# Performance work log

Measured on AMD Instinct MI355X. Metric: run time of the kernel, lower is better.

The kernel has to match this reference:

```python
import jax, jax.numpy as jnp
import numpy as np

N_NODES = 100000
N_EDGES = 1600000
IN_DIM = 256
HID = 64
OUT_DIM = 1
N_GRAPHS = 100


def setup_inputs() -> dict:
    key = jax.random.key(0)
    ks = jax.random.split(key, 12)
    x = jax.random.normal(ks[0], (N_NODES, IN_DIM), dtype=jnp.float32)
    edge_index = jax.random.randint(ks[1], (2, N_EDGES), 0, N_NODES, dtype=jnp.int64 if jax.config.read('jax_enable_x64') else jnp.int32)
    batch = jnp.sort(jax.random.randint(ks[2], (N_NODES,), 0, N_GRAPHS, dtype=jnp.int32))
    def lin(k, fan_in, fan_out):
        bound = 1.0 / np.sqrt(fan_in)
        kw, kb = jax.random.split(k)
        W = jax.random.uniform(kw, (fan_in, fan_out), minval=-bound, maxval=bound, dtype=jnp.float32)
        b = jax.random.uniform(kb, (fan_out,), minval=-bound, maxval=bound, dtype=jnp.float32)
        return W, b
    W1, b1 = lin(ks[3], IN_DIM, HID)
    W2, b2 = lin(ks[4], HID, HID)
    W3, b3 = lin(ks[5], HID, HID)
    Wl, bl = lin(ks[6], HID, OUT_DIM)
    return {"x": x, "edge_index": edge_index, "batch": batch,
            "W1": W1, "b1": b1, "W2": W2, "b2": b2, "W3": W3, "b3": b3,
            "Wl": Wl, "bl": bl}


def _gcn_layer(h, src, dst, norm, W, b):
    # PyG GCNConv: h' = scatter_add(norm * (h @ W)[src] -> dst) + b
    h = h @ W                                   # [N, F_out]
    msg = h[src] * norm[:, None]                # [E+N, F_out] irregular gather
    agg = jax.ops.segment_sum(msg, dst, num_segments=N_NODES)
    return agg + b


def reference(x, edge_index, batch, W1, b1, W2, b2, W3, b3, Wl, bl):
    # add self loops (static shape) as GCNConv does by default
    loops = jnp.arange(N_NODES, dtype=edge_index.dtype)
    src = jnp.concatenate([edge_index[0], loops])  # [E+N]
    dst = jnp.concatenate([edge_index[1], loops])  # [E+N]
    # symmetric normalization: deg over targets incl. self loops
    deg = jax.ops.segment_sum(jnp.ones_like(dst, dtype=x.dtype), dst, num_segments=N_NODES)
    dinv = jnp.where(deg > 0, jax.lax.rsqrt(deg), 0.0)
    norm = dinv[src] * dinv[dst]                # [E+N]

    h = jax.nn.relu(_gcn_layer(x, src, dst, norm, W1, b1))
    h = jax.nn.relu(_gcn_layer(h, src, dst, norm, W2, b2))
    h = _gcn_layer(h, src, dst, norm, W3, b3)   # last conv: no relu

    # global_add_pool over graphs; dropout is identity at inference
    pooled = jax.ops.segment_sum(h, batch, num_segments=N_GRAPHS)  # [G, HID]
    return pooled @ Wl + bl                     # [G, 1]
```

## Files before the change

kernel.cpp:

```cpp
#include <hip/hip_runtime.h>

#define N_NODES 100000
#define N_EDGES 1600000
#define IN_DIM 256
#define HID 64
#define N_GRAPHS 100
#define BSHIFT 8
#define NBUCK 391
#define CHUNK 4096
#define BCAP 5120

typedef __attribute__((ext_vector_type(8))) short short8;
typedef __attribute__((ext_vector_type(8))) unsigned short us8;
typedef __attribute__((ext_vector_type(4))) float floatx4;

__device__ __forceinline__ unsigned short f2b(float f) {
    unsigned int u = __float_as_uint(f);
    unsigned int r = (u + 0x7FFFu + ((u >> 16) & 1u)) >> 16;
    return (unsigned short)r;
}
__device__ __forceinline__ float b2f(unsigned short b) {
    return __uint_as_float(((unsigned int)b) << 16);
}


__global__ void k_prep(const float* __restrict__ W1, const float* __restrict__ W2,
                       const float* __restrict__ W3, const float* __restrict__ Wl,
                       const float* __restrict__ b3,
                       unsigned short* __restrict__ wt1, unsigned short* __restrict__ wt2,
                       float* __restrict__ w3l,
                       int* __restrict__ bcnt, float* __restrict__ partial) {
    int i = blockIdx.x * 256 + threadIdx.x;
    if (i < IN_DIM * HID) {
        int k = i >> 6, n = i & 63;
        wt1[n * IN_DIM + k] = f2b(W1[i]);
    }
    if (i < HID * HID) {
        int k = i >> 6, n = i & 63;
        wt2[n * HID + k] = f2b(W2[i]);
    }
    if (i < NBUCK) bcnt[i] = 0;
    if (i < N_GRAPHS * 256) partial[i] = 0.f;
    if (blockIdx.x == 0) {
        int t = threadIdx.x;
        if (t < HID) {
            float s = 0.f;
            for (int n = 0; n < HID; ++n) s += W3[t * HID + n] * Wl[n];
            w3l[t] = s;
        } else if (t == HID) {
            float s = 0.f;
            for (int n = 0; n < HID; ++n) s += b3[n] * Wl[n];
            w3l[HID] = s;
        }
    }
}


__global__ __launch_bounds__(256) void k_scatter(const int* __restrict__ src,
                                                 const int* __restrict__ dst,
                                                 int* __restrict__ bcnt,
                                                 int* __restrict__ ebuckF) {
    __shared__ int lc[NBUCK];
    const int b = blockIdx.x, t = threadIdx.x;
    for (int i = t; i < NBUCK; i += 256) lc[i] = 0;
    __syncthreads();
    const int base = b * CHUNK;
    int pk[16], bk[16], rk[16];
#pragma unroll
    for (int i = 0; i < 16; ++i) {
        int e = base + i * 256 + t;
        rk[i] = -1;
        if (e < N_EDGES) {
            int s = src[e], d = dst[e];
            bk[i] = d >> BSHIFT;
            pk[i] = (s << BSHIFT) | (d & 255);
            rk[i] = atomicAdd(&lc[bk[i]], 1);
        }
    }
    __syncthreads();
    for (int i = t; i < NBUCK; i += 256)
        lc[i] = lc[i] ? atomicAdd(&bcnt[i], lc[i]) : 0;
    __syncthreads();
#pragma unroll
    for (int i = 0; i < 16; ++i)
        if (rk[i] >= 0) {
            int p = lc[bk[i]] + rk[i];
            if (p < BCAP) ebuckF[bk[i] * BCAP + p] = pk[i];
        }
}


__global__ __launch_bounds__(256) void k_degfill(const int* __restrict__ bcnt,
                                                 const int* __restrict__ ebuckF,
                                                 int* __restrict__ deg,
                                                 float* __restrict__ dinv,
                                                 int* __restrict__ rowptr,
                                                 int* __restrict__ colF) {
    __shared__ int ld[256];
    __shared__ int sA[256];
    __shared__ int lf[256];
    const int b = blockIdx.x, t = threadIdx.x;
    const int cnt = min(bcnt[b], BCAP);
    const int ebase = b * BCAP;
    ld[t] = 1;
    __syncthreads();
    for (int j = t; j < cnt; j += 256) atomicAdd(&ld[ebuckF[ebase + j] & 255], 1);
    __syncthreads();
    const int node = (b << BSHIFT) + t;
    const int dg = ld[t];
    if (node < N_NODES) {
        deg[node] = dg;
        dinv[node] = rsqrtf((float)dg);
    }
    const int c = (node < N_NODES) ? dg - 1 : 0;
    sA[t] = c;
    __syncthreads();
    for (int off = 1; off < 256; off <<= 1) {
        int u = (t >= off) ? sA[t - off] : 0;
        __syncthreads();
        sA[t] += u;
        __syncthreads();
    }
    const int pos = ebase + sA[t] - c;
    if (node < N_NODES) rowptr[node] = pos;
    lf[t] = pos;
    __syncthreads();
    for (int j = t; j < cnt; j += 256) {
        int v = ebuckF[ebase + j];
        int p = atomicAdd(&lf[v & 255], 1);
        colF[p] = v >> BSHIFT;
    }
}


__global__ __launch_bounds__(256) void k_gemm1(const float* __restrict__ X,
                                               const unsigned short* __restrict__ Wt,
                                               const float* __restrict__ dinv,
                                               unsigned short* __restrict__ Tb) {
    __shared__ unsigned short Wb[64][264];
    const int t = threadIdx.x;
    const int lane = t & 63, wv = t >> 6;
    const int fl = lane & 15, quad = lane >> 4;
    const int r0 = blockIdx.x * 64;

    for (int g = t; g < 64 * 32; g += 256) {
        int n = g >> 5, kc8 = g & 31;
        *(us8*)&Wb[n][kc8 * 8] = *(const us8*)(Wt + n * IN_DIM + kc8 * 8);
    }

    const int arow = r0 + wv * 16 + fl;
    const bool valid = arow < N_NODES;
    const float* xp = X + (size_t)(valid ? arow : 0) * IN_DIM;

    floatx4 acc[4];
#pragma unroll
    for (int j = 0; j < 4; ++j) acc[j] = (floatx4){0.f, 0.f, 0.f, 0.f};

    __syncthreads();

#pragma unroll
    for (int kc = 0; kc < IN_DIM; kc += 32) {
        float4 x0 = make_float4(0.f, 0.f, 0.f, 0.f);
        float4 x1 = make_float4(0.f, 0.f, 0.f, 0.f);
        if (valid) {
            x0 = *(const float4*)(xp + kc + quad * 8);
            x1 = *(const float4*)(xp + kc + quad * 8 + 4);
        }
        short8 a;
        a[0] = (short)f2b(x0.x); a[1] = (short)f2b(x0.y);
        a[2] = (short)f2b(x0.z); a[3] = (short)f2b(x0.w);
        a[4] = (short)f2b(x1.x); a[5] = (short)f2b(x1.y);
        a[6] = (short)f2b(x1.z); a[7] = (short)f2b(x1.w);
#pragma unroll
        for (int ct = 0; ct < 4; ++ct) {
            short8 b = *(const short8*)&Wb[ct * 16 + fl][kc + quad * 8];
            acc[ct] = __builtin_amdgcn_mfma_f32_16x16x32_bf16(a, b, acc[ct], 0, 0, 0);
        }
    }

    int rbase = r0 + wv * 16 + quad * 4;
#pragma unroll
    for (int r = 0; r < 4; ++r) {
        int row = rbase + r;
        if (row < N_NODES) {
            float di = dinv[row];
#pragma unroll
            for (int ct = 0; ct < 4; ++ct)
                Tb[(size_t)row * HID + ct * 16 + fl] = f2b(di * acc[ct][r]);
        }
    }
}


__global__ __launch_bounds__(256) void k_gemm2(const unsigned short* __restrict__ Xin,
                                               const unsigned short* __restrict__ Wt,
                                               const float* __restrict__ dinv,
                                               unsigned short* __restrict__ Tb) {
    __shared__ unsigned short Wb[64][72];
    const int t = threadIdx.x;
    const int lane = t & 63, wv = t >> 6;
    const int fl = lane & 15, quad = lane >> 4;
    const int r0 = blockIdx.x * 64;

    for (int g = t; g < 64 * 8; g += 256) {
        int n = g >> 3, kc8 = g & 7;
        *(us8*)&Wb[n][kc8 * 8] = *(const us8*)(Wt + n * HID + kc8 * 8);
    }

    const int arow = r0 + wv * 16 + fl;
    const bool valid = arow < N_NODES;
    const unsigned short* xp = Xin + (size_t)(valid ? arow : 0) * HID;

    floatx4 acc[4];
#pragma unroll
    for (int j = 0; j < 4; ++j) acc[j] = (floatx4){0.f, 0.f, 0.f, 0.f};

    __syncthreads();

#pragma unroll
    for (int kc = 0; kc < HID; kc += 32) {
        short8 a = (short8){0, 0, 0, 0, 0, 0, 0, 0};
        if (valid) a = *(const short8*)(xp + kc + quad * 8);
#pragma unroll
        for (int ct = 0; ct < 4; ++ct) {
            short8 b = *(const short8*)&Wb[ct * 16 + fl][kc + quad * 8];
            acc[ct] = __builtin_amdgcn_mfma_f32_16x16x32_bf16(a, b, acc[ct], 0, 0, 0);
        }
    }

    int rbase = r0 + wv * 16 + quad * 4;
#pragma unroll
    for (int r = 0; r < 4; ++r) {
        int row = rbase + r;
        if (row < N_NODES) {
            float di = dinv[row];
#pragma unroll
            for (int ct = 0; ct < 4; ++ct)
                Tb[(size_t)row * HID + ct * 16 + fl] = f2b(di * acc[ct][r]);
        }
    }
}


__global__ __launch_bounds__(1024) void k_agg(const unsigned short* __restrict__ Tb,
                                              const int* __restrict__ rowptr,
                                              const int* __restrict__ deg,
                                              const float* __restrict__ dinv,
                                              const int* __restrict__ col,
                                              const float* __restrict__ bias,
                                              unsigned short* __restrict__ Hb) {
    int lane = threadIdx.x & 63;
    int node = blockIdx.x * 16 + (threadIdx.x >> 6);
    int grp = lane >> 3, fl = lane & 7;
    int e = __builtin_amdgcn_readfirstlane(rowptr[node]);
    int end = e + __builtin_amdgcn_readfirstlane(deg[node]) - 1;
    float a0 = 0.f, a1 = 0.f, a2 = 0.f, a3 = 0.f;
    float a4 = 0.f, a5 = 0.f, a6 = 0.f, a7 = 0.f;
    for (; e + 16 <= end; e += 16) {
        int s0 = col[e + grp];
        int s1 = col[e + 8 + grp];
        us8 t0 = *(const us8*)(Tb + (size_t)s0 * HID + fl * 8);
        us8 t1 = *(const us8*)(Tb + (size_t)s1 * HID + fl * 8);
        a0 += b2f(t0[0]) + b2f(t1[0]); a1 += b2f(t0[1]) + b2f(t1[1]);
        a2 += b2f(t0[2]) + b2f(t1[2]); a3 += b2f(t0[3]) + b2f(t1[3]);
        a4 += b2f(t0[4]) + b2f(t1[4]); a5 += b2f(t0[5]) + b2f(t1[5]);
        a6 += b2f(t0[6]) + b2f(t1[6]); a7 += b2f(t0[7]) + b2f(t1[7]);
    }
    for (; e + 8 <= end; e += 8) {
        int s = col[e + grp];
        us8 tv = *(const us8*)(Tb + (size_t)s * HID + fl * 8);
        a0 += b2f(tv[0]); a1 += b2f(tv[1]); a2 += b2f(tv[2]); a3 += b2f(tv[3]);
        a4 += b2f(tv[4]); a5 += b2f(tv[5]); a6 += b2f(tv[6]); a7 += b2f(tv[7]);
    }
    if (e + grp < end) {
        int s = col[e + grp];
        us8 tv = *(const us8*)(Tb + (size_t)s * HID + fl * 8);
        a0 += b2f(tv[0]); a1 += b2f(tv[1]); a2 += b2f(tv[2]); a3 += b2f(tv[3]);
        a4 += b2f(tv[4]); a5 += b2f(tv[5]); a6 += b2f(tv[6]); a7 += b2f(tv[7]);
    }
    a0 += __shfl_xor(a0, 8);  a1 += __shfl_xor(a1, 8);
    a2 += __shfl_xor(a2, 8);  a3 += __shfl_xor(a3, 8);
    a4 += __shfl_xor(a4, 8);  a5 += __shfl_xor(a5, 8);
    a6 += __shfl_xor(a6, 8);  a7 += __shfl_xor(a7, 8);
    a0 += __shfl_xor(a0, 16); a1 += __shfl_xor(a1, 16);
    a2 += __shfl_xor(a2, 16); a3 += __shfl_xor(a3, 16);
    a4 += __shfl_xor(a4, 16); a5 += __shfl_xor(a5, 16);
    a6 += __shfl_xor(a6, 16); a7 += __shfl_xor(a7, 16);
    a0 += __shfl_xor(a0, 32); a1 += __shfl_xor(a1, 32);
    a2 += __shfl_xor(a2, 32); a3 += __shfl_xor(a3, 32);
    a4 += __shfl_xor(a4, 32); a5 += __shfl_xor(a5, 32);
    a6 += __shfl_xor(a6, 32); a7 += __shfl_xor(a7, 32);
    us8 sv = *(const us8*)(Tb + (size_t)node * HID + fl * 8);
    a0 += b2f(sv[0]); a1 += b2f(sv[1]); a2 += b2f(sv[2]); a3 += b2f(sv[3]);
    a4 += b2f(sv[4]); a5 += b2f(sv[5]); a6 += b2f(sv[6]); a7 += b2f(sv[7]);
    float di = dinv[node];
    float4 b0 = *(const float4*)(bias + fl * 8);
    float4 b1v = *(const float4*)(bias + fl * 8 + 4);
    a0 = fmaxf(fmaf(di, a0, b0.x), 0.f);
    a1 = fmaxf(fmaf(di, a1, b0.y), 0.f);
    a2 = fmaxf(fmaf(di, a2, b0.z), 0.f);
    a3 = fmaxf(fmaf(di, a3, b0.w), 0.f);
    a4 = fmaxf(fmaf(di, a4, b1v.x), 0.f);
    a5 = fmaxf(fmaf(di, a5, b1v.y), 0.f);
    a6 = fmaxf(fmaf(di, a6, b1v.z), 0.f);
    a7 = fmaxf(fmaf(di, a7, b1v.w), 0.f);
    if (grp == 0) {
        us8 o;
        o[0] = f2b(a0); o[1] = f2b(a1); o[2] = f2b(a2); o[3] = f2b(a3);
        o[4] = f2b(a4); o[5] = f2b(a5); o[6] = f2b(a6); o[7] = f2b(a7);
        *(us8*)(Hb + (size_t)node * HID + fl * 8) = o;
    }
}


__global__ __launch_bounds__(1024) void k_agg_z(const unsigned short* __restrict__ Tb,
                                                const int* __restrict__ rowptr,
                                                const int* __restrict__ deg,
                                                const float* __restrict__ dinv,
                                                const int* __restrict__ col,
                                                const float* __restrict__ bias,
                                                const float* __restrict__ w3l,
                                                float* __restrict__ z) {
    int lane = threadIdx.x & 63;
    int node = blockIdx.x * 16 + (threadIdx.x >> 6);
    int grp = lane >> 3, fl = lane & 7;
    int e = __builtin_amdgcn_readfirstlane(rowptr[node]);
    int end = e + __builtin_amdgcn_readfirstlane(deg[node]) - 1;
    float a0 = 0.f, a1 = 0.f, a2 = 0.f, a3 = 0.f;
    float a4 = 0.f, a5 = 0.f, a6 = 0.f, a7 = 0.f;
    for (; e + 16 <= end; e += 16) {
        int s0 = col[e + grp];
        int s1 = col[e + 8 + grp];
        us8 t0 = *(const us8*)(Tb + (size_t)s0 * HID + fl * 8);
        us8 t1 = *(const us8*)(Tb + (size_t)s1 * HID + fl * 8);
        a0 += b2f(t0[0]) + b2f(t1[0]); a1 += b2f(t0[1]) + b2f(t1[1]);
        a2 += b2f(t0[2]) + b2f(t1[2]); a3 += b2f(t0[3]) + b2f(t1[3]);
        a4 += b2f(t0[4]) + b2f(t1[4]); a5 += b2f(t0[5]) + b2f(t1[5]);
        a6 += b2f(t0[6]) + b2f(t1[6]); a7 += b2f(t0[7]) + b2f(t1[7]);
    }
    for (; e + 8 <= end; e += 8) {
        int s = col[e + grp];
        us8 tv = *(const us8*)(Tb + (size_t)s * HID + fl * 8);
        a0 += b2f(tv[0]); a1 += b2f(tv[1]); a2 += b2f(tv[2]); a3 += b2f(tv[3]);
        a4 += b2f(tv[4]); a5 += b2f(tv[5]); a6 += b2f(tv[6]); a7 += b2f(tv[7]);
    }
    if (e + grp < end) {
        int s = col[e + grp];
        us8 tv = *(const us8*)(Tb + (size_t)s * HID + fl * 8);
        a0 += b2f(tv[0]); a1 += b2f(tv[1]); a2 += b2f(tv[2]); a3 += b2f(tv[3]);
        a4 += b2f(tv[4]); a5 += b2f(tv[5]); a6 += b2f(tv[6]); a7 += b2f(tv[7]);
    }
    a0 += __shfl_xor(a0, 8);  a1 += __shfl_xor(a1, 8);
    a2 += __shfl_xor(a2, 8);  a3 += __shfl_xor(a3, 8);
    a4 += __shfl_xor(a4, 8);  a5 += __shfl_xor(a5, 8);
    a6 += __shfl_xor(a6, 8);  a7 += __shfl_xor(a7, 8);
    a0 += __shfl_xor(a0, 16); a1 += __shfl_xor(a1, 16);
    a2 += __shfl_xor(a2, 16); a3 += __shfl_xor(a3, 16);
    a4 += __shfl_xor(a4, 16); a5 += __shfl_xor(a5, 16);
    a6 += __shfl_xor(a6, 16); a7 += __shfl_xor(a7, 16);
    a0 += __shfl_xor(a0, 32); a1 += __shfl_xor(a1, 32);
    a2 += __shfl_xor(a2, 32); a3 += __shfl_xor(a3, 32);
    a4 += __shfl_xor(a4, 32); a5 += __shfl_xor(a5, 32);
    a6 += __shfl_xor(a6, 32); a7 += __shfl_xor(a7, 32);
    us8 sv = *(const us8*)(Tb + (size_t)node * HID + fl * 8);
    a0 += b2f(sv[0]); a1 += b2f(sv[1]); a2 += b2f(sv[2]); a3 += b2f(sv[3]);
    a4 += b2f(sv[4]); a5 += b2f(sv[5]); a6 += b2f(sv[6]); a7 += b2f(sv[7]);
    float di = dinv[node];
    float4 b0 = *(const float4*)(bias + fl * 8);
    float4 b1v = *(const float4*)(bias + fl * 8 + 4);
    a0 = fmaxf(fmaf(di, a0, b0.x), 0.f);
    a1 = fmaxf(fmaf(di, a1, b0.y), 0.f);
    a2 = fmaxf(fmaf(di, a2, b0.z), 0.f);
    a3 = fmaxf(fmaf(di, a3, b0.w), 0.f);
    a4 = fmaxf(fmaf(di, a4, b1v.x), 0.f);
    a5 = fmaxf(fmaf(di, a5, b1v.y), 0.f);
    a6 = fmaxf(fmaf(di, a6, b1v.z), 0.f);
    a7 = fmaxf(fmaf(di, a7, b1v.w), 0.f);
    float4 w0 = *(const float4*)(w3l + fl * 8);
    float4 w1v = *(const float4*)(w3l + fl * 8 + 4);
    float s = a0 * w0.x + a1 * w0.y + a2 * w0.z + a3 * w0.w +
              a4 * w1v.x + a5 * w1v.y + a6 * w1v.z + a7 * w1v.w;
    s += __shfl_xor(s, 1);
    s += __shfl_xor(s, 2);
    s += __shfl_xor(s, 4);
    if (lane == 0) z[node] = di * s;
}

__global__ __launch_bounds__(256) void k_aggpool_s(const float* __restrict__ z,
                                                   const int* __restrict__ rowptr,
                                                   const int* __restrict__ deg,
                                                   const float* __restrict__ dinv,
                                                   const int* __restrict__ col,
                                                   const float* __restrict__ w3l,
                                                   const int* __restrict__ batch,
                                                   float* __restrict__ partial) {
    int i = blockIdx.x * 256 + threadIdx.x;
    if (i >= N_NODES) return;
    int e = rowptr[i];
    int end = e + deg[i] - 1;
    float s0 = z[i], s1 = 0.f, s2 = 0.f, s3 = 0.f;
    for (; e + 4 <= end; e += 4) {
        s0 += z[col[e]];
        s1 += z[col[e + 1]];
        s2 += z[col[e + 2]];
        s3 += z[col[e + 3]];
    }
    for (; e < end; ++e) s0 += z[col[e]];
    float s = w3l[HID] + dinv[i] * (s0 + s1 + s2 + s3);
    atomicAdd(&partial[batch[i] * 256 + (blockIdx.x & 255)], s);
}

__global__ void k_pool_reduce(const float* __restrict__ partial,
                              const float* __restrict__ bl,
                              float* __restrict__ out) {
    int g = blockIdx.x, t = threadIdx.x;
    float s = partial[g * 256 + t];
    s += __shfl_xor(s, 32);
    s += __shfl_xor(s, 16);
    s += __shfl_xor(s, 8);
    s += __shfl_xor(s, 4);
    s += __shfl_xor(s, 2);
    s += __shfl_xor(s, 1);
    __shared__ float ws[4];
    if ((t & 63) == 0) ws[t >> 6] = s;
    __syncthreads();
    if (t == 0) out[g] = bl[0] + ws[0] + ws[1] + ws[2] + ws[3];
}

extern "C" void kernel_launch(void* const* d_in, const int* in_sizes, int n_in,
                              void* d_out, int out_size, void* d_ws, size_t ws_size,
                              hipStream_t stream) {
    const float* x     = (const float*)d_in[0];
    const int*   ei    = (const int*)d_in[1];
    const int*   batch = (const int*)d_in[2];
    const float* W1    = (const float*)d_in[3];
    const float* b1    = (const float*)d_in[4];
    const float* W2    = (const float*)d_in[5];
    const float* b2    = (const float*)d_in[6];
    const float* W3    = (const float*)d_in[7];
    const float* b3    = (const float*)d_in[8];
    const float* Wl    = (const float*)d_in[9];
    const float* bl    = (const float*)d_in[10];
    float* out = (float*)d_out;

    char* p = (char*)d_ws;
    unsigned short* tb = (unsigned short*)p; p += (size_t)N_NODES * HID * 2;
    unsigned short* hB = (unsigned short*)p; p += (size_t)N_NODES * HID * 2;
    int*   colF    = (int*)p;   p += (size_t)NBUCK * BCAP * 4;
    int*   ebuckF  = (int*)p;   p += (size_t)NBUCK * BCAP * 4;
    int*   deg     = (int*)p;   p += (size_t)N_NODES * 4;
    float* dinv    = (float*)p; p += (size_t)N_NODES * 4;
    int*   rowptr  = (int*)p;   p += (size_t)N_NODES * 4;
    float* z       = (float*)p; p += (size_t)N_NODES * 4;
    int*   bcnt    = (int*)p;   p += (NBUCK + 1) * 4;
    float* partial = (float*)p; p += (size_t)N_GRAPHS * 256 * 4;
    unsigned short* wt1 = (unsigned short*)p; p += (size_t)IN_DIM * HID * 2;
    unsigned short* wt2 = (unsigned short*)p; p += (size_t)HID * HID * 2;
    float* w3l     = (float*)p; p += 128 * 4;

    const int* src  = ei;
    const int* dstp = ei + N_EDGES;

    const int nb = (N_NODES + 255) / 256;
    const int cb = (N_EDGES + CHUNK - 1) / CHUNK;
    const int gemm_blocks = (N_NODES + 63) / 64;
    const int agg_blocks = (N_NODES + 15) / 16;

    k_prep<<<128, 256, 0, stream>>>(W1, W2, W3, Wl, b3, wt1, wt2, w3l, bcnt, partial);
    k_scatter<<<cb, 256, 0, stream>>>(src, dstp, bcnt, ebuckF);
    k_degfill<<<NBUCK, 256, 0, stream>>>(bcnt, ebuckF, deg, dinv, rowptr, colF);

    k_gemm1<<<gemm_blocks, 256, 0, stream>>>(x, wt1, dinv, tb);
    k_agg<<<agg_blocks, 1024, 0, stream>>>(tb, rowptr, deg, dinv, colF, b1, hB);
    k_gemm2<<<gemm_blocks, 256, 0, stream>>>(hB, wt2, dinv, tb);
    k_agg_z<<<agg_blocks, 1024, 0, stream>>>(tb, rowptr, deg, dinv, colF, b2, w3l, z);

    k_aggpool_s<<<nb, 256, 0, stream>>>(z, rowptr, deg, dinv, colF, w3l, batch, partial);
    k_pool_reduce<<<N_GRAPHS, 256, 0, stream>>>(partial, bl, out);
}
```

Measured before the change: 365.6 us.

## Replace bucketed CSR build with fixed-capacity per-node adjacency and fuse agg with gemm2

Replaces the two-pass bucket scatter and degree/prefix-sum fill with a single atomic scatter into a fixed 64-slot adjacency list per destination node, computing the normalisation from the counts wherever it is needed. It also fuses the layer-1 aggregation with the layer-2 GEMM in one kernel that stages 16 aggregated rows in shared memory for a single wave's MFMA. This drops two graph-build kernels and the separate GEMM launch with its round trip of hidden features. In exchange it uses a global atomic per edge, edges beyond 64 per node are silently dropped, and the MFMA stage runs on only one wave per block.

```diff
diff --git a/kernel.cpp b/kernel.cpp
--- a/kernel.cpp
+++ b/kernel.cpp
@@ -5,10 +5,7 @@
 #define IN_DIM 256
 #define HID 64
 #define N_GRAPHS 100
-#define BSHIFT 8
-#define NBUCK 391
-#define CHUNK 4096
-#define BCAP 5120
+#define NCAP 64
 
 typedef __attribute__((ext_vector_type(8))) short short8;
 typedef __attribute__((ext_vector_type(8))) unsigned short us8;
@@ -24,12 +21,16 @@
 }
 
 
-__global__ void k_prep(const float* __restrict__ W1, const float* __restrict__ W2,
-                       const float* __restrict__ W3, const float* __restrict__ Wl,
-                       const float* __restrict__ b3,
-                       unsigned short* __restrict__ wt1, unsigned short* __restrict__ wt2,
-                       float* __restrict__ w3l,
-                       int* __restrict__ bcnt, float* __restrict__ partial) {
+__global__ __launch_bounds__(256) void k_prep(const float* __restrict__ W1,
+                                              const float* __restrict__ W2,
+                                              const float* __restrict__ W3,
+                                              const float* __restrict__ Wl,
+                                              const float* __restrict__ b3,
+                                              unsigned short* __restrict__ wt1,
+                                              unsigned short* __restrict__ wt2,
+                                              float* __restrict__ w3l,
+                                              int* __restrict__ ncnt,
+                                              float* __restrict__ partial) {
     int i = blockIdx.x * 256 + threadIdx.x;
     if (i < IN_DIM * HID) {
         int k = i >> 6, n = i & 63;
@@ -39,7 +40,7 @@
         int k = i >> 6, n = i & 63;
         wt2[n * HID + k] = f2b(W2[i]);
     }
-    if (i < NBUCK) bcnt[i] = 0;
+    if (i < N_NODES) ncnt[i] = 0;
     if (i < N_GRAPHS * 256) partial[i] = 0.f;
     if (blockIdx.x == 0) {
         int t = threadIdx.x;
@@ -56,86 +57,26 @@
 }
 
 
-__global__ __launch_bounds__(256) void k_scatter(const int* __restrict__ src,
-                                                 const int* __restrict__ dst,
-                                                 int* __restrict__ bcnt,
-                                                 int* __restrict__ ebuckF) {
-    __shared__ int lc[NBUCK];
-    const int b = blockIdx.x, t = threadIdx.x;
-    for (int i = t; i < NBUCK; i += 256) lc[i] = 0;
-    __syncthreads();
-    const int base = b * CHUNK;
-    int pk[16], bk[16], rk[16];
-#pragma unroll
-    for (int i = 0; i < 16; ++i) {
-        int e = base + i * 256 + t;
-        rk[i] = -1;
+__global__ __launch_bounds__(256) void k_dscatter(const int* __restrict__ src,
+                                                  const int* __restrict__ dst,
+                                                  int* __restrict__ ncnt,
+                                                  int* __restrict__ col) {
+    int base = blockIdx.x * 1024 + threadIdx.x;
+#pragma unroll
+    for (int i = 0; i < 4; ++i) {
+        int e = base + i * 256;
         if (e < N_EDGES) {
-            int s = src[e], d = dst[e];
-            bk[i] = d >> BSHIFT;
-            pk[i] = (s << BSHIFT) | (d & 255);
-            rk[i] = atomicAdd(&lc[bk[i]], 1);
-        }
-    }
-    __syncthreads();
-    for (int i = t; i < NBUCK; i += 256)
-        lc[i] = lc[i] ? atomicAdd(&bcnt[i], lc[i]) : 0;
-    __syncthreads();
-#pragma unroll
-    for (int i = 0; i < 16; ++i)
-        if (rk[i] >= 0) {
-            int p = lc[bk[i]] + rk[i];
-            if (p < BCAP) ebuckF[bk[i] * BCAP + p] = pk[i];
-        }
-}
-
-
-__global__ __launch_bounds__(256) void k_degfill(const int* __restrict__ bcnt,
-                                                 const int* __restrict__ ebuckF,
-                                                 int* __restrict__ deg,
-                                                 float* __restrict__ dinv,
-                                                 int* __restrict__ rowptr,
-                                                 int* __restrict__ colF) {
-    __shared__ int ld[256];
-    __shared__ int sA[256];
-    __shared__ int lf[256];
-    const int b = blockIdx.x, t = threadIdx.x;
-    const int cnt = min(bcnt[b], BCAP);
-    const int ebase = b * BCAP;
-    ld[t] = 1;
-    __syncthreads();
-    for (int j = t; j < cnt; j += 256) atomicAdd(&ld[ebuckF[ebase + j] & 255], 1);
-    __syncthreads();
-    const int node = (b << BSHIFT) + t;
-    const int dg = ld[t];
-    if (node < N_NODES) {
-        deg[node] = dg;
-        dinv[node] = rsqrtf((float)dg);
-    }
-    const int c = (node < N_NODES) ? dg - 1 : 0;
-    sA[t] = c;
-    __syncthreads();
-    for (int off = 1; off < 256; off <<= 1) {
-        int u = (t >= off) ? sA[t - off] : 0;
-        __syncthreads();
-        sA[t] += u;
-        __syncthreads();
-    }
-    const int pos = ebase + sA[t] - c;
-    if (node < N_NODES) rowptr[node] = pos;
-    lf[t] = pos;
-    __syncthreads();
-    for (int j = t; j < cnt; j += 256) {
-        int v = ebuckF[ebase + j];
-        int p = atomicAdd(&lf[v & 255], 1);
-        colF[p] = v >> BSHIFT;
+            int d = dst[e];
+            int slot = atomicAdd(&ncnt[d], 1);
+            if (slot < NCAP) col[(size_t)d * NCAP + slot] = src[e];
+        }
     }
 }
 
 
 __global__ __launch_bounds__(256) void k_gemm1(const float* __restrict__ X,
                                                const unsigned short* __restrict__ Wt,
-                                               const float* __restrict__ dinv,
+                                               const int* __restrict__ ncnt,
                                                unsigned short* __restrict__ Tb) {
     __shared__ unsigned short Wb[64][264];
     const int t = threadIdx.x;
@@ -183,7 +124,7 @@
     for (int r = 0; r < 4; ++r) {
         int row = rbase + r;
         if (row < N_NODES) {
-            float di = dinv[row];
+            float di = rsqrtf((float)(min(ncnt[row], NCAP) + 1));
 #pragma unroll
             for (int ct = 0; ct < 4; ++ct)
                 Tb[(size_t)row * HID + ct * 16 + fl] = f2b(di * acc[ct][r]);
@@ -192,68 +133,124 @@
 }
 
 
-__global__ __launch_bounds__(256) void k_gemm2(const unsigned short* __restrict__ Xin,
-                                               const unsigned short* __restrict__ Wt,
-                                               const float* __restrict__ dinv,
-                                               unsigned short* __restrict__ Tb) {
+__global__ __launch_bounds__(1024) void k_aggmm2(const unsigned short* __restrict__ Tb,
+                                                 const int* __restrict__ ncnt,
+                                                 const int* __restrict__ col,
+                                                 const float* __restrict__ bias,
+                                                 const unsigned short* __restrict__ Wt,
+                                                 unsigned short* __restrict__ Tb2) {
     __shared__ unsigned short Wb[64][72];
+    __shared__ unsigned short Hs[16][72];
     const int t = threadIdx.x;
     const int lane = t & 63, wv = t >> 6;
-    const int fl = lane & 15, quad = lane >> 4;
-    const int r0 = blockIdx.x * 64;
-
-    for (int g = t; g < 64 * 8; g += 256) {
+    const int grp = lane >> 3, fl8 = lane & 7;
+
+    for (int g = t; g < 64 * 8; g += 1024) {
         int n = g >> 3, kc8 = g & 7;
         *(us8*)&Wb[n][kc8 * 8] = *(const us8*)(Wt + n * HID + kc8 * 8);
     }
 
-    const int arow = r0 + wv * 16 + fl;
-    const bool valid = arow < N_NODES;
-    const unsigned short* xp = Xin + (size_t)(valid ? arow : 0) * HID;
-
-    floatx4 acc[4];
-#pragma unroll
-    for (int j = 0; j < 4; ++j) acc[j] = (floatx4){0.f, 0.f, 0.f, 0.f};
-
+    const int node = blockIdx.x * 16 + wv;
+    const int cnt = min(__builtin_amdgcn_readfirstlane(ncnt[node]), NCAP);
+    int e = node * NCAP;
+    const int end = e + cnt;
+    float a0 = 0.f, a1 = 0.f, a2 = 0.f, a3 = 0.f;
+    float a4 = 0.f, a5 = 0.f, a6 = 0.f, a7 = 0.f;
+    for (; e + 16 <= end; e += 16) {
+        int s0 = col[e + grp];
+        int s1 = col[e + 8 + grp];
+        us8 t0 = *(const us8*)(Tb + (size_t)s0 * HID + fl8 * 8);
+        us8 t1 = *(const us8*)(Tb + (size_t)s1 * HID + fl8 * 8);
+        a0 += b2f(t0[0]) + b2f(t1[0]); a1 += b2f(t0[1]) + b2f(t1[1]);
+        a2 += b2f(t0[2]) + b2f(t1[2]); a3 += b2f(t0[3]) + b2f(t1[3]);
+        a4 += b2f(t0[4]) + b2f(t1[4]); a5 += b2f(t0[5]) + b2f(t1[5]);
+        a6 += b2f(t0[6]) + b2f(t1[6]); a7 += b2f(t0[7]) + b2f(t1[7]);
+    }
+    for (; e + 8 <= end; e += 8) {
+        int s = col[e + grp];
+        us8 tv = *(const us8*)(Tb + (size_t)s * HID + fl8 * 8);
+        a0 += b2f(tv[0]); a1 += b2f(tv[1]); a2 += b2f(tv[2]); a3 += b2f(tv[3]);
+        a4 += b2f(tv[4]); a5 += b2f(tv[5]); a6 += b2f(tv[6]); a7 += b2f(tv[7]);
+    }
+    if (e + grp < end) {
+        int s = col[e + grp];
+        us8 tv = *(const us8*)(Tb + (size_t)s * HID + fl8 * 8);
+        a0 += b2f(tv[0]); a1 += b2f(tv[1]); a2 += b2f(tv[2]); a3 += b2f(tv[3]);
+        a4 += b2f(tv[4]); a5 += b2f(tv[5]); a6 += b2f(tv[6]); a7 += b2f(tv[7]);
+    }
+    a0 += __shfl_xor(a0, 8);  a1 += __shfl_xor(a1, 8);
+    a2 += __shfl_xor(a2, 8);  a3 += __shfl_xor(a3, 8);
+    a4 += __shfl_xor(a4, 8);  a5 += __shfl_xor(a5, 8);
+    a6 += __shfl_xor(a6, 8);  a7 += __shfl_xor(a7, 8);
+    a0 += __shfl_xor(a0, 16); a1 += __shfl_xor(a1, 16);
+    a2 += __shfl_xor(a2, 16); a3 += __shfl_xor(a3, 16);
+    a4 += __shfl_xor(a4, 16); a5 += __shfl_xor(a5, 16);
+    a6 += __shfl_xor(a6, 16); a7 += __shfl_xor(a7, 16);
+    a0 += __shfl_xor(a0, 32); a1 += __shfl_xor(a1, 32);
+    a2 += __shfl_xor(a2, 32); a3 += __shfl_xor(a3, 32);
+    a4 += __shfl_xor(a4, 32); a5 += __shfl_xor(a5, 32);
+    a6 += __shfl_xor(a6, 32); a7 += __shfl_xor(a7, 32);
+    us8 sv = *(const us8*)(Tb + (size_t)node * HID + fl8 * 8);
+    a0 += b2f(sv[0]); a1 += b2f(sv[1]); a2 += b2f(sv[2]); a3 += b2f(sv[3]);
+    a4 += b2f(sv[4]); a5 += b2f(sv[5]); a6 += b2f(sv[6]); a7 += b2f(sv[7]);
+    float di = rsqrtf((float)(cnt + 1));
+    float4 b0 = *(const float4*)(bias + fl8 * 8);
+    float4 b1v = *(const float4*)(bias + fl8 * 8 + 4);
+    a0 = fmaxf(fmaf(di, a0, b0.x), 0.f);
+    a1 = fmaxf(fmaf(di, a1, b0.y), 0.f);
+    a2 = fmaxf(fmaf(di, a2, b0.z), 0.f);
+    a3 = fmaxf(fmaf(di, a3, b0.w), 0.f);
+    a4 = fmaxf(fmaf(di, a4, b1v.x), 0.f);
+    a5 = fmaxf(fmaf(di, a5, b1v.y), 0.f);
+    a6 = fmaxf(fmaf(di, a6, b1v.z), 0.f);
+    a7 = fmaxf(fmaf(di, a7, b1v.w), 0.f);
+    if (grp == 0) {
+        us8 o;
+        o[0] = f2b(a0); o[1] = f2b(a1); o[2] = f2b(a2); o[3] = f2b(a3);
+        o[4] = f2b(a4); o[5] = f2b(a5); o[6] = f2b(a6); o[7] = f2b(a7);
+        *(us8*)&Hs[wv][fl8 * 8] = o;
+    }
     __syncthreads();
 
-#pragma unroll
-    for (int kc = 0; kc < HID; kc += 32) {
-        short8 a = (short8){0, 0, 0, 0, 0, 0, 0, 0};
-        if (valid) a = *(const short8*)(xp + kc + quad * 8);
-#pragma unroll
-        for (int ct = 0; ct < 4; ++ct) {
-            short8 b = *(const short8*)&Wb[ct * 16 + fl][kc + quad * 8];
-            acc[ct] = __builtin_amdgcn_mfma_f32_16x16x32_bf16(a, b, acc[ct], 0, 0, 0);
-        }
-    }
-
-    int rbase = r0 + wv * 16 + quad * 4;
-#pragma unroll
-    for (int r = 0; r < 4; ++r) {
-        int row = rbase + r;
-        if (row < N_NODES) {
-            float di = dinv[row];
+    if (wv == 0) {
+        const int fl = lane & 15, quad = lane >> 4;
+        floatx4 acc[4];
+#pragma unroll
+        for (int j = 0; j < 4; ++j) acc[j] = (floatx4){0.f, 0.f, 0.f, 0.f};
+#pragma unroll
+        for (int kc = 0; kc < HID; kc += 32) {
+            short8 a = *(const short8*)&Hs[fl][kc + quad * 8];
+#pragma unroll
+            for (int ct = 0; ct < 4; ++ct) {
+                short8 b = *(const short8*)&Wb[ct * 16 + fl][kc + quad * 8];
+                acc[ct] = __builtin_amdgcn_mfma_f32_16x16x32_bf16(a, b, acc[ct], 0, 0, 0);
+            }
+        }
+        int rbase = blockIdx.x * 16 + quad * 4;
+#pragma unroll
+        for (int r = 0; r < 4; ++r) {
+            int row = rbase + r;
+            float di2 = rsqrtf((float)(min(ncnt[row], NCAP) + 1));
 #pragma unroll
             for (int ct = 0; ct < 4; ++ct)
-                Tb[(size_t)row * HID + ct * 16 + fl] = f2b(di * acc[ct][r]);
-        }
-    }
-}
-
-
-__global__ __launch_bounds__(1024) void k_agg(const unsigned short* __restrict__ Tb,
-                                              const int* __restrict__ rowptr,
-                                              const int* __restrict__ deg,
-                                              const float* __restrict__ dinv,
-                                              const int* __restrict__ col,
-                                              const float* __restrict__ bias,
-                                              unsigned short* __restrict__ Hb) {
+                Tb2[(size_t)row * HID + ct * 16 + fl] = f2b(di2 * acc[ct][r]);
+        }
+    }
+}
+
+
+__global__ __launch_bounds__(1024) void k_agg_z(const unsigned short* __restrict__ Tb,
+                                                const int* __restrict__ ncnt,
+                                                const int* __restrict__ col,
+                                                const float* __restrict__ bias,
+                                                const float* __restrict__ w3l,
+                                                float* __restrict__ z) {
     int lane = threadIdx.x & 63;
     int node = blockIdx.x * 16 + (threadIdx.x >> 6);
     int grp = lane >> 3, fl = lane & 7;
-    int e = __builtin_amdgcn_readfirstlane(rowptr[node]);
-    int end = e + __builtin_amdgcn_readfirstlane(deg[node]) - 1;
+    const int cnt = min(__builtin_amdgcn_readfirstlane(ncnt[node]), NCAP);
+    int e = node * NCAP;
+    const int end = e + cnt;
     float a0 = 0.f, a1 = 0.f, a2 = 0.f, a3 = 0.f;
     float a4 = 0.f, a5 = 0.f, a6 = 0.f, a7 = 0.f;
     for (; e + 16 <= end; e += 16) {
@@ -293,79 +290,7 @@
     us8 sv = *(const us8*)(Tb + (size_t)node * HID + fl * 8);
     a0 += b2f(sv[0]); a1 += b2f(sv[1]); a2 += b2f(sv[2]); a3 += b2f(sv[3]);
     a4 += b2f(sv[4]); a5 += b2f(sv[5]); a6 += b2f(sv[6]); a7 += b2f(sv[7]);
-    float di = dinv[node];
-    float4 b0 = *(const float4*)(bias + fl * 8);
-    float4 b1v = *(const float4*)(bias + fl * 8 + 4);
-    a0 = fmaxf(fmaf(di, a0, b0.x), 0.f);
-    a1 = fmaxf(fmaf(di, a1, b0.y), 0.f);
-    a2 = fmaxf(fmaf(di, a2, b0.z), 0.f);
-    a3 = fmaxf(fmaf(di, a3, b0.w), 0.f);
-    a4 = fmaxf(fmaf(di, a4, b1v.x), 0.f);
-    a5 = fmaxf(fmaf(di, a5, b1v.y), 0.f);
-    a6 = fmaxf(fmaf(di, a6, b1v.z), 0.f);
-    a7 = fmaxf(fmaf(di, a7, b1v.w), 0.f);
-    if (grp == 0) {
-        us8 o;
-        o[0] = f2b(a0); o[1] = f2b(a1); o[2] = f2b(a2); o[3] = f2b(a3);
-        o[4] = f2b(a4); o[5] = f2b(a5); o[6] = f2b(a6); o[7] = f2b(a7);
-        *(us8*)(Hb + (size_t)node * HID + fl * 8) = o;
-    }
-}
-
-
-__global__ __launch_bounds__(1024) void k_agg_z(const unsigned short* __restrict__ Tb,
-                                                const int* __restrict__ rowptr,
-                                                const int* __restrict__ deg,
-                                                const float* __restrict__ dinv,
-                                                const int* __restrict__ col,
-                                                const float* __restrict__ bias,
-                                                const float* __restrict__ w3l,
-                                                float* __restrict__ z) {
-    int lane = threadIdx.x & 63;
-    int node = blockIdx.x * 16 + (threadIdx.x >> 6);
-    int grp = lane >> 3, fl = lane & 7;
-    int e = __builtin_amdgcn_readfirstlane(rowptr[node]);
-    int end = e + __builtin_amdgcn_readfirstlane(deg[node]) - 1;
-    float a0 = 0.f, a1 = 0.f, a2 = 0.f, a3 = 0.f;
-    float a4 = 0.f, a5 = 0.f, a6 = 0.f, a7 = 0.f;
-    for (; e + 16 <= end; e += 16) {
-        int s0 = col[e + grp];
-        int s1 = col[e + 8 + grp];
-        us8 t0 = *(const us8*)(Tb + (size_t)s0 * HID + fl * 8);
-        us8 t1 = *(const us8*)(Tb + (size_t)s1 * HID + fl * 8);
-        a0 += b2f(t0[0]) + b2f(t1[0]); a1 += b2f(t0[1]) + b2f(t1[1]);
-        a2 += b2f(t0[2]) + b2f(t1[2]); a3 += b2f(t0[3]) + b2f(t1[3]);
-        a4 += b2f(t0[4]) + b2f(t1[4]); a5 += b2f(t0[5]) + b2f(t1[5]);
-        a6 += b2f(t0[6]) + b2f(t1[6]); a7 += b2f(t0[7]) + b2f(t1[7]);
-    }
-    for (; e + 8 <= end; e += 8) {
-        int s = col[e + grp];
-        us8 tv = *(const us8*)(Tb + (size_t)s * HID + fl * 8);
-        a0 += b2f(tv[0]); a1 += b2f(tv[1]); a2 += b2f(tv[2]); a3 += b2f(tv[3]);
-        a4 += b2f(tv[4]); a5 += b2f(tv[5]); a6 += b2f(tv[6]); a7 += b2f(tv[7]);
-    }
-    if (e + grp < end) {
-        int s = col[e + grp];
-        us8 tv = *(const us8*)(Tb + (size_t)s * HID + fl * 8);
-        a0 += b2f(tv[0]); a1 += b2f(tv[1]); a2 += b2f(tv[2]); a3 += b2f(tv[3]);
-        a4 += b2f(tv[4]); a5 += b2f(tv[5]); a6 += b2f(tv[6]); a7 += b2f(tv[7]);
-    }
-    a0 += __shfl_xor(a0, 8);  a1 += __shfl_xor(a1, 8);
-    a2 += __shfl_xor(a2, 8);  a3 += __shfl_xor(a3, 8);
-    a4 += __shfl_xor(a4, 8);  a5 += __shfl_xor(a5, 8);
-    a6 += __shfl_xor(a6, 8);  a7 += __shfl_xor(a7, 8);
-    a0 += __shfl_xor(a0, 16); a1 += __shfl_xor(a1, 16);
-    a2 += __shfl_xor(a2, 16); a3 += __shfl_xor(a3, 16);
-    a4 += __shfl_xor(a4, 16); a5 += __shfl_xor(a5, 16);
-    a6 += __shfl_xor(a6, 16); a7 += __shfl_xor(a7, 16);
-    a0 += __shfl_xor(a0, 32); a1 += __shfl_xor(a1, 32);
-    a2 += __shfl_xor(a2, 32); a3 += __shfl_xor(a3, 32);
-    a4 += __shfl_xor(a4, 32); a5 += __shfl_xor(a5, 32);
-    a6 += __shfl_xor(a6, 32); a7 += __shfl_xor(a7, 32);
-    us8 sv = *(const us8*)(Tb + (size_t)node * HID + fl * 8);
-    a0 += b2f(sv[0]); a1 += b2f(sv[1]); a2 += b2f(sv[2]); a3 += b2f(sv[3]);
-    a4 += b2f(sv[4]); a5 += b2f(sv[5]); a6 += b2f(sv[6]); a7 += b2f(sv[7]);
-    float di = dinv[node];
+    float di = rsqrtf((float)(cnt + 1));
     float4 b0 = *(const float4*)(bias + fl * 8);
     float4 b1v = *(const float4*)(bias + fl * 8 + 4);
     a0 = fmaxf(fmaf(di, a0, b0.x), 0.f);
@@ -387,17 +312,16 @@
 }
 
 __global__ __launch_bounds__(256) void k_aggpool_s(const float* __restrict__ z,
-                                                   const int* __restrict__ rowptr,
-                                                   const int* __restrict__ deg,
-                                                   const float* __restrict__ dinv,
+                                                   const int* __restrict__ ncnt,
                                                    const int* __restrict__ col,
                                                    const float* __restrict__ w3l,
                                                    const int* __restrict__ batch,
                                                    float* __restrict__ partial) {
     int i = blockIdx.x * 256 + threadIdx.x;
     if (i >= N_NODES) return;
-    int e = rowptr[i];
-    int end = e + deg[i] - 1;
+    int cnt = min(ncnt[i], NCAP);
+    int e = i * NCAP;
+    int end = e + cnt;
     float s0 = z[i], s1 = 0.f, s2 = 0.f, s3 = 0.f;
     for (; e + 4 <= end; e += 4) {
         s0 += z[col[e]];
@@ -406,7 +330,8 @@
         s3 += z[col[e + 3]];
     }
     for (; e < end; ++e) s0 += z[col[e]];
-    float s = w3l[HID] + dinv[i] * (s0 + s1 + s2 + s3);
+    float di = rsqrtf((float)(cnt + 1));
+    float s = w3l[HID] + di * (s0 + s1 + s2 + s3);
     atomicAdd(&partial[batch[i] * 256 + (blockIdx.x & 255)], s);
 }
 
@@ -446,13 +371,9 @@
     char* p = (char*)d_ws;
     unsigned short* tb = (unsigned short*)p; p += (size_t)N_NODES * HID * 2;
     unsigned short* hB = (unsigned short*)p; p += (size_t)N_NODES * HID * 2;
-    int*   colF    = (int*)p;   p += (size_t)NBUCK * BCAP * 4;
-    int*   ebuckF  = (int*)p;   p += (size_t)NBUCK * BCAP * 4;
-    int*   deg     = (int*)p;   p += (size_t)N_NODES * 4;
-    float* dinv    = (float*)p; p += (size_t)N_NODES * 4;
-    int*   rowptr  = (int*)p;   p += (size_t)N_NODES * 4;
+    int*   col     = (int*)p;   p += (size_t)N_NODES * NCAP * 4;
+    int*   ncnt    = (int*)p;   p += (size_t)N_NODES * 4;
     float* z       = (float*)p; p += (size_t)N_NODES * 4;
-    int*   bcnt    = (int*)p;   p += (NBUCK + 1) * 4;
     float* partial = (float*)p; p += (size_t)N_GRAPHS * 256 * 4;
     unsigned short* wt1 = (unsigned short*)p; p += (size_t)IN_DIM * HID * 2;
     unsigned short* wt2 = (unsigned short*)p; p += (size_t)HID * HID * 2;
@@ -462,19 +383,17 @@
     const int* dstp = ei + N_EDGES;
 
     const int nb = (N_NODES + 255) / 256;
-    const int cb = (N_EDGES + CHUNK - 1) / CHUNK;
+    const int sb = (N_EDGES + 1023) / 1024;
     const int gemm_blocks = (N_NODES + 63) / 64;
-    const int agg_blocks = (N_NODES + 15) / 16;
-
-    k_prep<<<128, 256, 0, stream>>>(W1, W2, W3, Wl, b3, wt1, wt2, w3l, bcnt, partial);
-    k_scatter<<<cb, 256, 0, stream>>>(src, dstp, bcnt, ebuckF);
-    k_degfill<<<NBUCK, 256, 0, stream>>>(bcnt, ebuckF, deg, dinv, rowptr, colF);
-
-    k_gemm1<<<gemm_blocks, 256, 0, stream>>>(x, wt1, dinv, tb);
-    k_agg<<<agg_blocks, 1024, 0, stream>>>(tb, rowptr, deg, dinv, colF, b1, hB);
-    k_gemm2<<<gemm_blocks, 256, 0, stream>>>(hB, wt2, dinv, tb);
-    k_agg_z<<<agg_blocks, 1024, 0, stream>>>(tb, rowptr, deg, dinv, colF, b2, w3l, z);
-
-    k_aggpool_s<<<nb, 256, 0, stream>>>(z, rowptr, deg, dinv, colF, w3l, batch, partial);
+    const int agg_blocks = N_NODES / 16;
+
+    k_prep<<<nb, 256, 0, stream>>>(W1, W2, W3, Wl, b3, wt1, wt2, w3l, ncnt, partial);
+    k_dscatter<<<sb, 256, 0, stream>>>(src, dstp, ncnt, col);
+
+    k_gemm1<<<gemm_blocks, 256, 0, stream>>>(x, wt1, ncnt, tb);
+    k_aggmm2<<<agg_blocks, 1024, 0, stream>>>(tb, ncnt, col, b1, wt2, hB);
+    k_agg_z<<<agg_blocks, 1024, 0, stream>>>(hB, ncnt, col, b2, w3l, z);
+
+    k_aggpool_s<<<nb, 256, 0, stream>>>(z, ncnt, col, w3l, batch, partial);
     k_pool_reduce<<<N_GRAPHS, 256, 0, stream>>>(partial, bl, out);
 }
```

New measurement: 419.1 us. 14.6% more time.

## Fuse layer-1 aggregation with layer-2 GEMM via shared-memory tile

Applied to the files above, without the earlier changes.

Merges the first aggregation kernel and the second 64x64 GEMM into one kernel. Each 1024-thread block aggregates 16 nodes into a shared-memory tile, then one wave runs MFMA against W2 held in LDS and writes the scaled bf16 result. This drops one launch and the global write and read of the intermediate hidden activations. In exchange it adds a block-wide barrier, and 15 of the 16 waves sit idle during the GEMM phase.

```diff
diff --git a/kernel.cpp b/kernel.cpp
--- a/kernel.cpp
+++ b/kernel.cpp
@@ -192,75 +192,35 @@
 }
 
 
-__global__ __launch_bounds__(256) void k_gemm2(const unsigned short* __restrict__ Xin,
-                                               const unsigned short* __restrict__ Wt,
-                                               const float* __restrict__ dinv,
-                                               unsigned short* __restrict__ Tb) {
+__global__ __launch_bounds__(1024) void k_aggmm2(const unsigned short* __restrict__ Tb,
+                                                 const int* __restrict__ rowptr,
+                                                 const int* __restrict__ deg,
+                                                 const float* __restrict__ dinv,
+                                                 const int* __restrict__ col,
+                                                 const float* __restrict__ bias,
+                                                 const unsigned short* __restrict__ Wt,
+                                                 unsigned short* __restrict__ Tb2) {
     __shared__ unsigned short Wb[64][72];
+    __shared__ unsigned short Hs[16][72];
     const int t = threadIdx.x;
     const int lane = t & 63, wv = t >> 6;
-    const int fl = lane & 15, quad = lane >> 4;
-    const int r0 = blockIdx.x * 64;
-
-    for (int g = t; g < 64 * 8; g += 256) {
+    const int grp = lane >> 3, fl8 = lane & 7;
+
+    for (int g = t; g < 64 * 8; g += 1024) {
         int n = g >> 3, kc8 = g & 7;
         *(us8*)&Wb[n][kc8 * 8] = *(const us8*)(Wt + n * HID + kc8 * 8);
     }
 
-    const int arow = r0 + wv * 16 + fl;
-    const bool valid = arow < N_NODES;
-    const unsigned short* xp = Xin + (size_t)(valid ? arow : 0) * HID;
-
-    floatx4 acc[4];
-#pragma unroll
-    for (int j = 0; j < 4; ++j) acc[j] = (floatx4){0.f, 0.f, 0.f, 0.f};
-
-    __syncthreads();
-
-#pragma unroll
-    for (int kc = 0; kc < HID; kc += 32) {
-        short8 a = (short8){0, 0, 0, 0, 0, 0, 0, 0};
-        if (valid) a = *(const short8*)(xp + kc + quad * 8);
-#pragma unroll
-        for (int ct = 0; ct < 4; ++ct) {
-            short8 b = *(const short8*)&Wb[ct * 16 + fl][kc + quad * 8];
-            acc[ct] = __builtin_amdgcn_mfma_f32_16x16x32_bf16(a, b, acc[ct], 0, 0, 0);
-        }
-    }
-
-    int rbase = r0 + wv * 16 + quad * 4;
-#pragma unroll
-    for (int r = 0; r < 4; ++r) {
-        int row = rbase + r;
-        if (row < N_NODES) {
-            float di = dinv[row];
-#pragma unroll
-            for (int ct = 0; ct < 4; ++ct)
-                Tb[(size_t)row * HID + ct * 16 + fl] = f2b(di * acc[ct][r]);
-        }
-    }
-}
-
-
-__global__ __launch_bounds__(1024) void k_agg(const unsigned short* __restrict__ Tb,
-                                              const int* __restrict__ rowptr,
-                                              const int* __restrict__ deg,
-                                              const float* __restrict__ dinv,
-                                              const int* __restrict__ col,
-                                              const float* __restrict__ bias,
-                                              unsigned short* __restrict__ Hb) {
-    int lane = threadIdx.x & 63;
-    int node = blockIdx.x * 16 + (threadIdx.x >> 6);
-    int grp = lane >> 3, fl = lane & 7;
+    const int node = blockIdx.x * 16 + wv;
     int e = __builtin_amdgcn_readfirstlane(rowptr[node]);
-    int end = e + __builtin_amdgcn_readfirstlane(deg[node]) - 1;
+    const int end = e + __builtin_amdgcn_readfirstlane(deg[node]) - 1;
     float a0 = 0.f, a1 = 0.f, a2 = 0.f, a3 = 0.f;
     float a4 = 0.f, a5 = 0.f, a6 = 0.f, a7 = 0.f;
     for (; e + 16 <= end; e += 16) {
         int s0 = col[e + grp];
         int s1 = col[e + 8 + grp];
-        us8 t0 = *(const us8*)(Tb + (size_t)s0 * HID + fl * 8);
-        us8 t1 = *(const us8*)(Tb + (size_t)s1 * HID + fl * 8);
+        us8 t0 = *(const us8*)(Tb + (size_t)s0 * HID + fl8 * 8);
+        us8 t1 = *(const us8*)(Tb + (size_t)s1 * HID + fl8 * 8);
         a0 += b2f(t0[0]) + b2f(t1[0]); a1 += b2f(t0[1]) + b2f(t1[1]);
         a2 += b2f(t0[2]) + b2f(t1[2]); a3 += b2f(t0[3]) + b2f(t1[3]);
         a4 += b2f(t0[4]) + b2f(t1[4]); a5 += b2f(t0[5]) + b2f(t1[5]);
@@ -268,13 +228,13 @@
     }
     for (; e + 8 <= end; e += 8) {
         int s = col[e + grp];
-        us8 tv = *(const us8*)(Tb + (size_t)s * HID + fl * 8);
+        us8 tv = *(const us8*)(Tb + (size_t)s * HID + fl8 * 8);
         a0 += b2f(tv[0]); a1 += b2f(tv[1]); a2 += b2f(tv[2]); a3 += b2f(tv[3]);
         a4 += b2f(tv[4]); a5 += b2f(tv[5]); a6 += b2f(tv[6]); a7 += b2f(tv[7]);
     }
     if (e + grp < end) {
         int s = col[e + grp];
-        us8 tv = *(const us8*)(Tb + (size_t)s * HID + fl * 8);
+        us8 tv = *(const us8*)(Tb + (size_t)s * HID + fl8 * 8);
         a0 += b2f(tv[0]); a1 += b2f(tv[1]); a2 += b2f(tv[2]); a3 += b2f(tv[3]);
         a4 += b2f(tv[4]); a5 += b2f(tv[5]); a6 += b2f(tv[6]); a7 += b2f(tv[7]);
     }
@@ -290,12 +250,12 @@
     a2 += __shfl_xor(a2, 32); a3 += __shfl_xor(a3, 32);
     a4 += __shfl_xor(a4, 32); a5 += __shfl_xor(a5, 32);
     a6 += __shfl_xor(a6, 32); a7 += __shfl_xor(a7, 32);
-    us8 sv = *(const us8*)(Tb + (size_t)node * HID + fl * 8);
+    us8 sv = *(const us8*)(Tb + (size_t)node * HID + fl8 * 8);
     a0 += b2f(sv[0]); a1 += b2f(sv[1]); a2 += b2f(sv[2]); a3 += b2f(sv[3]);
     a4 += b2f(sv[4]); a5 += b2f(sv[5]); a6 += b2f(sv[6]); a7 += b2f(sv[7]);
     float di = dinv[node];
-    float4 b0 = *(const float4*)(bias + fl * 8);
-    float4 b1v = *(const float4*)(bias + fl * 8 + 4);
+    float4 b0 = *(const float4*)(bias + fl8 * 8);
+    float4 b1v = *(const float4*)(bias + fl8 * 8 + 4);
     a0 = fmaxf(fmaf(di, a0, b0.x), 0.f);
     a1 = fmaxf(fmaf(di, a1, b0.y), 0.f);
     a2 = fmaxf(fmaf(di, a2, b0.z), 0.f);
@@ -308,7 +268,33 @@
         us8 o;
         o[0] = f2b(a0); o[1] = f2b(a1); o[2] = f2b(a2); o[3] = f2b(a3);
         o[4] = f2b(a4); o[5] = f2b(a5); o[6] = f2b(a6); o[7] = f2b(a7);
-        *(us8*)(Hb + (size_t)node * HID + fl * 8) = o;
+        *(us8*)&Hs[wv][fl8 * 8] = o;
+    }
+    __syncthreads();
+
+    if (wv == 0) {
+        const int fl = lane & 15, quad = lane >> 4;
+        floatx4 acc[4];
+#pragma unroll
+        for (int j = 0; j < 4; ++j) acc[j] = (floatx4){0.f, 0.f, 0.f, 0.f};
+#pragma unroll
+        for (int kc = 0; kc < HID; kc += 32) {
+            short8 a = *(const short8*)&Hs[fl][kc + quad * 8];
+#pragma unroll
+            for (int ct = 0; ct < 4; ++ct) {
+                short8 b = *(const short8*)&Wb[ct * 16 + fl][kc + quad * 8];
+                acc[ct] = __builtin_amdgcn_mfma_f32_16x16x32_bf16(a, b, acc[ct], 0, 0, 0);
+            }
+        }
+        int rbase = blockIdx.x * 16 + quad * 4;
+#pragma unroll
+        for (int r = 0; r < 4; ++r) {
+            int row = rbase + r;
+            float di2 = dinv[row];
+#pragma unroll
+            for (int ct = 0; ct < 4; ++ct)
+                Tb2[(size_t)row * HID + ct * 16 + fl] = f2b(di2 * acc[ct][r]);
+        }
     }
 }
 
@@ -464,16 +450,15 @@
     const int nb = (N_NODES + 255) / 256;
     const int cb = (N_EDGES + CHUNK - 1) / CHUNK;
     const int gemm_blocks = (N_NODES + 63) / 64;
-    const int agg_blocks = (N_NODES + 15) / 16;
+    const int agg_blocks = N_NODES / 16;
 
     k_prep<<<128, 256, 0, stream>>>(W1, W2, W3, Wl, b3, wt1, wt2, w3l, bcnt, partial);
     k_scatter<<<cb, 256, 0, stream>>>(src, dstp, bcnt, ebuckF);
     k_degfill<<<NBUCK, 256, 0, stream>>>(bcnt, ebuckF, deg, dinv, rowptr, colF);
 
     k_gemm1<<<gemm_blocks, 256, 0, stream>>>(x, wt1, dinv, tb);
-    k_agg<<<agg_blocks, 1024, 0, stream>>>(tb, rowptr, deg, dinv, colF, b1, hB);
-    k_gemm2<<<gemm_blocks, 256, 0, stream>>>(hB, wt2, dinv, tb);
-    k_agg_z<<<agg_blocks, 1024, 0, stream>>>(tb, rowptr, deg, dinv, colF, b2, w3l, z);
+    k_aggmm2<<<agg_blocks, 1024, 0, stream>>>(tb, rowptr, deg, dinv, colF, b1, wt2, hB);
+    k_agg_z<<<agg_blocks, 1024, 0, stream>>>(hB, rowptr, deg, dinv, colF, b2, w3l, z);
 
     k_aggpool_s<<<nb, 256, 0, stream>>>(z, rowptr, deg, dinv, colF, w3l, batch, partial);
     k_pool_reduce<<<N_GRAPHS, 256, 0, stream>>>(partial, bl, out);
```

After: 363.1 us. About the same (-0.7%).
